# Optimization experiments

Measured on AMD Instinct MI355X. Metric: run time of the kernel, lower is better.

Reference implementation:

```python
import jax, jax.numpy as jnp
import numpy as np

EPS = 1e-5


def setup_inputs() -> dict:
    key = jax.random.key(0)
    ks = jax.random.split(key, 16)
    N, P, K, D = 16, 1024, 16, 3
    Cf = 64      # out_features (lifted feature dim)
    Fin = 64     # feature_dim
    Cout = 128   # out_channels
    DM = 4       # depth multiplier
    Ccat = Cf + Fin  # 128
    s = 0.1
    return {
        'rep_pt': jax.random.normal(ks[0], (N, P, D), jnp.float32),
        'pts':    jax.random.normal(ks[1], (N, P, K, D), jnp.float32),
        'fts':    jax.random.normal(ks[2], (N, P, K, Fin), jnp.float32),
        'W_fc1':  jax.random.normal(ks[3], (Cf, D), jnp.float32) * s,
        'b_fc1':  jnp.zeros((Cf,), jnp.float32),
        'W_fc2':  jax.random.normal(ks[4], (Cf, Cf), jnp.float32) * s,
        'b_fc2':  jnp.zeros((Cf,), jnp.float32),
        'W_xconv': jax.random.normal(ks[5], (K * K, D, K), jnp.float32) * s,
        'b_xconv': jnp.zeros((K * K,), jnp.float32),
        'W_xfc1': jax.random.normal(ks[6], (K * K, K * K), jnp.float32) * s,
        'b_xfc1': jnp.zeros((K * K,), jnp.float32),
        'W_xfc2': jax.random.normal(ks[7], (K * K, K * K), jnp.float32) * s,
        'b_xfc2': jnp.zeros((K * K,), jnp.float32),
        'W_dw':   jax.random.normal(ks[8], (Ccat, DM, K), jnp.float32) * s,
        'b_dw':   jnp.zeros((Ccat * DM,), jnp.float32),
        'W_pw':   jax.random.normal(ks[9], (Cout, Ccat * DM), jnp.float32) * s,
        'b_pw':   jnp.zeros((Cout,), jnp.float32),
        'gamma':  jnp.ones((Cout,), jnp.float32),
        'beta':   jnp.zeros((Cout,), jnp.float32),
    }


def reference(rep_pt, pts, fts, W_fc1, b_fc1, W_fc2, b_fc2,
              W_xconv, b_xconv, W_xfc1, b_xfc1, W_xfc2, b_xfc2,
              W_dw, b_dw, W_pw, b_pw, gamma, beta):
    relu = jax.nn.relu
    N, P, K, _ = pts.shape

    # local coords around each representative point
    pts_local = pts - rep_pt[:, :, None, :]                       # (N,P,K,3)

    # feature lift: two FCs with relu
    h = relu(jnp.einsum('npkd,fd->npkf', pts_local, W_fc1) + b_fc1)
    fts_lifted = relu(jnp.einsum('npkf,gf->npkg', h, W_fc2) + b_fc2)  # (N,P,K,Cf)
    fts_cat = jnp.concatenate([fts_lifted, fts], axis=-1)         # (N,P,K,Ccat)

    # X-transform: conv2d kernel (1,K) over (N,3,P,K) -> (N,K^2,P,1), then 2 FCs
    X = relu(jnp.einsum('npkd,odk->npo', pts_local, W_xconv) + b_xconv)  # (N,P,K^2)
    X = relu(X @ W_xfc1.T + b_xfc1)
    X = X @ W_xfc2.T + b_xfc2                                     # linear
    X = X.reshape(N, P, K, K)

    # X-transformed features
    fts_X = jnp.einsum('npij,npjc->npic', X, fts_cat)             # (N,P,K,Ccat)

    # depthwise-separable conv with kernel (1,K): reduces K entirely
    x = fts_X.transpose(0, 3, 1, 2)                               # (N,Ccat,P,K)
    dw = jnp.einsum('ncpk,cmk->ncmp', x, W_dw)                    # (N,Ccat,DM,P)
    dw = dw.reshape(N, -1, P) + b_dw[None, :, None]               # (N,Ccat*DM,P)
    y = jnp.einsum('ncp,oc->nop', dw, W_pw) + b_pw[None, :, None] # (N,Cout,P)

    # batchnorm (training stats over N,P per channel), then relu
    mean = y.mean(axis=(0, 2), keepdims=True)
    var = y.var(axis=(0, 2), keepdims=True)
    y = (y - mean) * jax.lax.rsqrt(var + EPS)
    y = relu(gamma[None, :, None] * y + beta[None, :, None])

    return y.transpose(0, 2, 1)                                   # (N,P,Cout)
```

## Files before the change

### kernel.cpp

```cpp
#include <hip/hip_runtime.h>


#define NPTS 16384

typedef short  s16x8 __attribute__((ext_vector_type(8)));
typedef float  f32x4 __attribute__((ext_vector_type(4)));

__device__ inline unsigned short f2b(float f) {
    unsigned u = __builtin_bit_cast(unsigned, f);
    unsigned r = u + 0x7FFF + ((u >> 16) & 1);
    return (unsigned short)(r >> 16);
}
__device__ inline float b2f(unsigned short b) {
    return __builtin_bit_cast(float, (unsigned)b << 16);
}
__device__ inline unsigned cvtpk(float lo, float hi) {
    unsigned r;
    asm("v_cvt_pk_bf16_f32 %0, %1, %2" : "=v"(r) : "v"(lo), "v"(hi));
    return r;
}

#define MFMA(a,b,c) __builtin_amdgcn_mfma_f32_16x16x32_bf16((a),(b),(c),0,0,0)

__global__ __launch_bounds__(256) void kW_cvt(
    const float* __restrict__ Wxc, const float* __restrict__ Wx1,
    const float* __restrict__ Wx2, const float* __restrict__ Wf2,
    const float* __restrict__ Wpw, const float* __restrict__ Wf1,
    const float* __restrict__ bf1, const float* __restrict__ Wdw,
    unsigned short* __restrict__ Wpk, float* __restrict__ W1p,
    unsigned short* __restrict__ Wtb, float* __restrict__ acc)
{
    unsigned short* Wxcpk = Wpk;
    unsigned short* Wx1pk = Wpk + 16384;
    unsigned short* Wx2pk = Wpk + 81920;
    unsigned short* Wf2pk = Wpk + 147456;
    unsigned short* Wpwpk = Wpk + 151552;
    int idx = blockIdx.x * 256 + threadIdx.x;
    if (idx < 16384) {
        int e = idx & 7, ln = (idx >> 3) & 63, ks = (idx >> 9) & 1, ot = idx >> 10;
        int row = ot*16 + (ln & 15), k = ks*32 + (ln >> 4)*8 + e;
        Wxcpk[idx] = (k < 48) ? f2b(Wxc[row*48 + k]) : 0; return; }
    idx -= 16384;
    if (idx < 65536) {
        int e = idx & 7, ln = (idx >> 3) & 63, ks = (idx >> 9) & 7, ot = idx >> 12;
        int row = ot*16 + (ln & 15), k = ks*32 + (ln >> 4)*8 + e;
        Wx1pk[idx] = f2b(Wx1[row*256 + k]); return; }
    idx -= 65536;
    if (idx < 65536) {
        int e = idx & 7, ln = (idx >> 3) & 63, ks = (idx >> 9) & 7, ot = idx >> 12;
        int row = ot*16 + (ln & 15), k = ks*32 + (ln >> 4)*8 + e;
        Wx2pk[idx] = f2b(Wx2[row*256 + k]); return; }
    idx -= 65536;
    if (idx < 4096) {
        int e = idx & 7, ln = (idx >> 3) & 63, ks = (idx >> 9) & 1, ot = idx >> 10;
        int row = ot*16 + (ln & 15), k = ks*32 + (ln >> 4)*8 + e;
        Wf2pk[idx] = f2b(Wf2[row*64 + k]); return; }
    idx -= 4096;
    if (idx < 65536) {
        int e = idx & 7, ln = (idx >> 3) & 63, ks = (idx >> 9) & 15, ot = idx >> 13;
        int row = ot*16 + (ln & 15), k = ks*32 + (ln >> 4)*8 + e;
        Wpwpk[idx] = f2b(Wpw[row*512 + k]); return; }
    idx -= 65536;
    if (idx < 256)   { int f = idx >> 2, j = idx & 3;
        W1p[idx] = (j < 3) ? Wf1[f*3 + j] : bf1[f]; return; }
    idx -= 256;
    if (idx < 8192)  { int m = idx >> 11, rem = idx & 2047;
        int c = rem >> 4, k = rem & 15;
        Wtb[idx] = f2b(Wdw[(size_t)(c*4 + m)*16 + k]); return; }
    idx -= 8192;
    if (idx < 256)   { acc[idx] = 0.f; return; }
}

#define SX 264
__global__ __launch_bounds__(512) void kA_mfma(
    const float* __restrict__ rep, const float* __restrict__ pts,
    const unsigned short* __restrict__ Wpk,
    const float* __restrict__ bxc, const float* __restrict__ bx1,
    const float* __restrict__ bx2, unsigned short* __restrict__ X3b)
{
    const unsigned short* Wxcpk = Wpk;
    const unsigned short* Wx1pk = Wpk + 16384;
    const unsigned short* Wx2pk = Wpk + 81920;
    __shared__ __align__(16) unsigned short X1s[32*SX];
    __shared__ __align__(16) unsigned short X2s[32*SX];
    const int tid = threadIdx.x;
    const int w = tid >> 6, lane = tid & 63, cl = lane & 15, lg = lane >> 4;
    const int mw = w & 1, nw = w >> 1;
    const int base = blockIdx.x * 32;
    const int q = base + mw*16 + cl;
    f32x4 z = {0.f,0.f,0.f,0.f};

    float r0 = rep[q*3+0], r1 = rep[q*3+1], r2 = rep[q*3+2];
    s16x8 aa[2];
    #pragma unroll
    for (int ks = 0; ks < 2; ++ks) {
        uint4 au;
        #pragma unroll
        for (int e2 = 0; e2 < 4; ++e2) {
            float v[2];
            #pragma unroll
            for (int h = 0; h < 2; ++h) {
                int j = ks*32 + lg*8 + e2*2 + h;
                float vv = 0.f;
                if (j < 48) {
                    int d = j >> 4, kk = j & 15;
                    float rv = (d == 0) ? r0 : ((d == 1) ? r1 : r2);
                    vv = pts[(size_t)(q*16 + kk)*3 + d] - rv;
                }
                v[h] = vv;
            }
            ((unsigned*)&au)[e2] = cvtpk(v[0], v[1]);
        }
        aa[ks] = __builtin_bit_cast(s16x8, au);
    }

    {
        f32x4 acc[4] = {z,z,z,z};
        #pragma unroll
        for (int ks = 0; ks < 2; ++ks) {
            #pragma unroll
            for (int ct = 0; ct < 4; ++ct) {
                int ot = nw*4 + ct;
                s16x8 b = *(const s16x8*)&Wxcpk[((ot*2 + ks)*64 + lane)*8];
                acc[ct] = MFMA(aa[ks], b, acc[ct]);
            }
        }
        #pragma unroll
        for (int ct = 0; ct < 4; ++ct) {
            int o = nw*64 + ct*16 + cl;
            float bias = bxc[o];
            int rb = (mw*16 + lg*4)*SX + o;
            unsigned u0 = cvtpk(fmaxf(acc[ct][0]+bias,0.f), fmaxf(acc[ct][1]+bias,0.f));
            unsigned u1 = cvtpk(fmaxf(acc[ct][2]+bias,0.f), fmaxf(acc[ct][3]+bias,0.f));
            X1s[rb       ] = (unsigned short)u0;
            X1s[rb +   SX] = (unsigned short)(u0 >> 16);
            X1s[rb + 2*SX] = (unsigned short)u1;
            X1s[rb + 3*SX] = (unsigned short)(u1 >> 16);
        }
    }
    __syncthreads();

    {
        f32x4 acc[4] = {z,z,z,z};
        #pragma unroll
        for (int ks = 0; ks < 8; ++ks) {
            s16x8 a = *(const s16x8*)&X1s[(mw*16 + cl)*SX + ks*32 + lg*8];
            #pragma unroll
            for (int ct = 0; ct < 4; ++ct) {
                int ot = nw*4 + ct;
                s16x8 b = *(const s16x8*)&Wx1pk[((ot*8 + ks)*64 + lane)*8];
                acc[ct] = MFMA(a, b, acc[ct]);
            }
        }
        #pragma unroll
        for (int ct = 0; ct < 4; ++ct) {
            int o = nw*64 + ct*16 + cl;
            float bias = bx1[o];
            int rb = (mw*16 + lg*4)*SX + o;
            unsigned u0 = cvtpk(fmaxf(acc[ct][0]+bias,0.f), fmaxf(acc[ct][1]+bias,0.f));
            unsigned u1 = cvtpk(fmaxf(acc[ct][2]+bias,0.f), fmaxf(acc[ct][3]+bias,0.f));
            X2s[rb       ] = (unsigned short)u0;
            X2s[rb +   SX] = (unsigned short)(u0 >> 16);
            X2s[rb + 2*SX] = (unsigned short)u1;
            X2s[rb + 3*SX] = (unsigned short)(u1 >> 16);
        }
    }
    __syncthreads();

    {
        f32x4 acc[4] = {z,z,z,z};
        #pragma unroll
        for (int ks = 0; ks < 8; ++ks) {
            s16x8 a = *(const s16x8*)&X2s[(mw*16 + cl)*SX + ks*32 + lg*8];
            #pragma unroll
            for (int ct = 0; ct < 4; ++ct) {
                int ot = nw*4 + ct;
                s16x8 b = *(const s16x8*)&Wx2pk[((ot*8 + ks)*64 + lane)*8];
                acc[ct] = MFMA(a, b, acc[ct]);
            }
        }
        #pragma unroll
        for (int ct = 0; ct < 4; ++ct) {
            int o = nw*64 + ct*16 + cl;
            float bias = bx2[o];
            size_t rb = (size_t)(base + mw*16 + lg*4)*256 + o;
            unsigned u0 = cvtpk(acc[ct][0]+bias, acc[ct][1]+bias);
            unsigned u1 = cvtpk(acc[ct][2]+bias, acc[ct][3]+bias);
            X3b[rb      ] = (unsigned short)u0;
            X3b[rb + 256] = (unsigned short)(u0 >> 16);
            X3b[rb + 512] = (unsigned short)u1;
            X3b[rb + 768] = (unsigned short)(u1 >> 16);
        }
    }
}

#define SF 72
__global__ __launch_bounds__(256) void kB_mfma(
    const float* __restrict__ rep, const float* __restrict__ pts,
    const float* __restrict__ fts, const float* __restrict__ W1p,
    const unsigned short* __restrict__ Wpk, const float* __restrict__ bf2,
    const unsigned short* __restrict__ Wtb, const float* __restrict__ bdw,
    const unsigned short* __restrict__ X3b, unsigned short* __restrict__ dwb)
{
    const unsigned short* Wf2pk = Wpk + 147456;
    __shared__ __align__(16) unsigned short fcT[128*SF];
    const int tid = threadIdx.x;
    const int w = tid >> 6, lane = tid & 63, cl = lane & 15, lg = lane >> 4;
    const int p = blockIdx.x*4 + w;
    const int rw = w*16;

    const int frow = lane >> 2, fch = lane & 3;
    float4 fv[4];
    #pragma unroll
    for (int it = 0; it < 4; ++it)
        fv[it] = *(const float4*)&fts[((size_t)p*16 + frow)*64 + fch*4 + it*16];

    s16x8 xa = {0,0,0,0,0,0,0,0};
    if (lg < 2) xa = *(const s16x8*)&X3b[(size_t)p*256 + cl*16 + lg*8];

    const int row = p*16 + cl;
    float x0 = pts[(size_t)row*3+0] - rep[p*3+0];
    float x1 = pts[(size_t)row*3+1] - rep[p*3+1];
    float x2 = pts[(size_t)row*3+2] - rep[p*3+2];

    s16x8 hb[2];
    #pragma unroll
    for (int ks = 0; ks < 2; ++ks) {
        uint4 hu;
        #pragma unroll
        for (int e2 = 0; e2 < 4; ++e2) {
            int f0 = ks*32 + lg*8 + e2*2;
            float4 wa = *(const float4*)&W1p[f0*4];
            float4 wb = *(const float4*)&W1p[(f0+1)*4];
            float h0 = fmaxf(wa.w + wa.x*x0 + wa.y*x1 + wa.z*x2, 0.f);
            float h1 = fmaxf(wb.w + wb.x*x0 + wb.y*x1 + wb.z*x2, 0.f);
            ((unsigned*)&hu)[e2] = cvtpk(h0, h1);
        }
        hb[ks] = __builtin_bit_cast(s16x8, hu);
    }

    #pragma unroll
    for (int it = 0; it < 4; ++it) {
        int c0 = fch*4 + it*16;
        unsigned u0 = cvtpk(fv[it].x, fv[it].y);
        unsigned u1 = cvtpk(fv[it].z, fv[it].w);
        int rb = (64 + c0)*SF + rw + frow;
        fcT[rb       ] = (unsigned short)u0;
        fcT[rb +   SF] = (unsigned short)(u0 >> 16);
        fcT[rb + 2*SF] = (unsigned short)u1;
        fcT[rb + 3*SF] = (unsigned short)(u1 >> 16);
    }

    f32x4 z = {0.f,0.f,0.f,0.f};
    {
        f32x4 acc2[4] = {z,z,z,z};
        #pragma unroll
        for (int ks = 0; ks < 2; ++ks) {
            #pragma unroll
            for (int gt = 0; gt < 4; ++gt) {
                s16x8 a = *(const s16x8*)&Wf2pk[((gt*2 + ks)*64 + lane)*8];
                acc2[gt] = MFMA(a, hb[ks], acc2[gt]);
            }
        }
        #pragma unroll
        for (int gt = 0; gt < 4; ++gt) {
            int g0 = gt*16 + lg*4;
            unsigned u0 = cvtpk(fmaxf(acc2[gt][0]+bf2[g0+0],0.f),
                                fmaxf(acc2[gt][1]+bf2[g0+1],0.f));
            unsigned u1 = cvtpk(fmaxf(acc2[gt][2]+bf2[g0+2],0.f),
                                fmaxf(acc2[gt][3]+bf2[g0+3],0.f));
            int rb = g0*SF + rw + cl;
            fcT[rb       ] = (unsigned short)u0;
            fcT[rb +   SF] = (unsigned short)(u0 >> 16);
            fcT[rb + 2*SF] = (unsigned short)u1;
            fcT[rb + 3*SF] = (unsigned short)(u1 >> 16);
        }
    }

    #pragma unroll
    for (int ct = 0; ct < 8; ++ct) {
        int c = ct*16 + cl;
        s16x8 b = *(const s16x8*)&fcT[c*SF + rw + (lg & 1)*8];
        f32x4 fx = MFMA(xa, b, z);

        float4 b4 = *(const float4*)&bdw[c*4];
        float om[4];
        #pragma unroll
        for (int m = 0; m < 4; ++m) {
            ushort4 wu = *(const ushort4*)&Wtb[m*2048 + c*16 + lg*4];
            float s = fx[0]*b2f(wu.x) + fx[1]*b2f(wu.y)
                    + fx[2]*b2f(wu.z) + fx[3]*b2f(wu.w);
            s += __shfl_xor(s, 16);
            s += __shfl_xor(s, 32);
            om[m] = s + ((const float*)&b4)[m];
        }
        if (lg == 0) {
            unsigned u0 = cvtpk(om[0], om[1]);
            unsigned u1 = cvtpk(om[2], om[3]);
            uint2 pk; pk.x = u0; pk.y = u1;
            *(uint2*)&dwb[(size_t)p*512 + c*4] = pk;
        }
    }
}

__global__ __launch_bounds__(256) void kC_mfma(
    const unsigned short* __restrict__ dwb, const unsigned short* __restrict__ Wpk,
    const float* __restrict__ bpw, float* __restrict__ y,
    float* __restrict__ accS, float* __restrict__ accS2)
{
    const unsigned short* Wpwpk = Wpk + 151552;
    const int tid = threadIdx.x;
    const int w = tid >> 6, lane = tid & 63, cl = lane & 15, lg = lane >> 4;
    const int m0 = blockIdx.x*32 + (w & 1)*16;
    const int nh = w >> 1;
    f32x4 z = {0.f,0.f,0.f,0.f};
    f32x4 acc[4] = {z,z,z,z};
    for (int ks = 0; ks < 16; ++ks) {
        s16x8 a = *(const s16x8*)&dwb[(size_t)(m0 + cl)*512 + ks*32 + lg*8];
        #pragma unroll
        for (int ct = 0; ct < 4; ++ct) {
            int ot = nh*4 + ct;
            s16x8 b = *(const s16x8*)&Wpwpk[((ot*16 + ks)*64 + lane)*8];
            acc[ct] = MFMA(a, b, acc[ct]);
        }
    }
    #pragma unroll
    for (int ct = 0; ct < 4; ++ct) {
        int o = nh*64 + ct*16 + cl;
        float bias = bpw[o];
        float s1 = 0.f, s2 = 0.f;
        #pragma unroll
        for (int r = 0; r < 4; ++r) {
            float v = acc[ct][r] + bias;
            y[(size_t)(m0 + lg*4 + r)*128 + o] = v;
            s1 += v; s2 += v*v;
        }
        s1 += __shfl_xor(s1, 16); s2 += __shfl_xor(s2, 16);
        s1 += __shfl_xor(s1, 32); s2 += __shfl_xor(s2, 32);
        if (lg == 0) {
            atomicAdd(accS + o, s1);
            atomicAdd(accS2 + o, s2);
        }
    }
}

__global__ __launch_bounds__(256) void kE_final(
    const float* __restrict__ y, const float* __restrict__ accS,
    const float* __restrict__ accS2, const float* __restrict__ gamma,
    const float* __restrict__ beta, float* __restrict__ out)
{
    __shared__ float stl[256];
    const int tid = threadIdx.x;
    if (tid < 128) {
        float mean = accS[tid] * (1.f/NPTS);
        float var  = accS2[tid] * (1.f/NPTS) - mean*mean;
        float rstd = rsqrtf(var + 1e-5f);
        float sc = gamma[tid] * rstd;
        stl[tid] = sc;
        stl[128 + tid] = beta[tid] - mean*sc;
    }
    __syncthreads();
    const int idx = blockIdx.x*256 + tid;
    float4 v = ((const float4*)y)[idx];
    int o0 = (idx & 31) << 2;
    float4 sc = *(const float4*)&stl[o0];
    float4 sh = *(const float4*)&stl[128 + o0];
    float4 r;
    r.x = fmaxf(v.x*sc.x + sh.x, 0.f);
    r.y = fmaxf(v.y*sc.y + sh.y, 0.f);
    r.z = fmaxf(v.z*sc.z + sh.z, 0.f);
    r.w = fmaxf(v.w*sc.w + sh.w, 0.f);
    ((float4*)out)[idx] = r;
}

extern "C" void kernel_launch(void* const* d_in, const int* in_sizes, int n_in,
                              void* d_out, int out_size, void* d_ws, size_t ws_size,
                              hipStream_t stream) {
    const float* rep  = (const float*)d_in[0];
    const float* pts  = (const float*)d_in[1];
    const float* fts  = (const float*)d_in[2];
    const float* Wf1  = (const float*)d_in[3];
    const float* bf1  = (const float*)d_in[4];
    const float* Wf2  = (const float*)d_in[5];
    const float* bf2  = (const float*)d_in[6];
    const float* Wxc  = (const float*)d_in[7];
    const float* bxc  = (const float*)d_in[8];
    const float* Wx1  = (const float*)d_in[9];
    const float* bx1  = (const float*)d_in[10];
    const float* Wx2  = (const float*)d_in[11];
    const float* bx2  = (const float*)d_in[12];
    const float* Wdw  = (const float*)d_in[13];
    const float* bdw  = (const float*)d_in[14];
    const float* Wpw  = (const float*)d_in[15];
    const float* bpw  = (const float*)d_in[16];
    const float* gam  = (const float*)d_in[17];
    const float* bet  = (const float*)d_in[18];

    unsigned short* X3b = (unsigned short*)d_ws;
    unsigned short* dwb = X3b + (size_t)NPTS*256;
    float* y   = (float*)(dwb + (size_t)NPTS*512);
    float* acc = y + (size_t)NPTS*128;
    unsigned short* Wpk = (unsigned short*)(acc + 256);
    float* W1p = (float*)(Wpk + 217088);
    unsigned short* Wtb = (unsigned short*)(W1p + 256);

    kW_cvt<<<882, 256, 0, stream>>>(Wxc, Wx1, Wx2, Wf2, Wpw, Wf1, bf1, Wdw,
                                    Wpk, W1p, Wtb, acc);
    kA_mfma<<<NPTS/32, 512, 0, stream>>>(rep, pts, Wpk, bxc, bx1, bx2, X3b);
    kB_mfma<<<NPTS/4, 256, 0, stream>>>(rep, pts, fts, W1p, Wpk, bf2, Wtb, bdw, X3b, dwb);
    kC_mfma<<<NPTS/32, 256, 0, stream>>>(dwb, Wpk, bpw, y, acc, acc + 128);
    kE_final<<<(NPTS*128/4)/256, 256, 0, stream>>>(y, acc, acc + 128, gam, bet, (float*)d_out);
}
```

Baseline: 116.8 us.

## Store depthwise output in MFMA-packed layout and pre-BN activations as bf16

kB now writes its depthwise result directly into the fragment-packed order kC consumes, so each lane of kC loads its A operand with one contiguous vector read. The intermediate y written by kC and read by kE is stored in bf16 instead of fp32, halving that round trip's memory traffic. Batch-norm statistics are still accumulated from fp32 values, but normalization is applied to bf16-rounded values, which adds rounding error.

```diff
diff --git a/kernel.cpp b/kernel.cpp
--- a/kernel.cpp
+++ b/kernel.cpp
@@ -200,7 +200,7 @@
     const float* __restrict__ fts, const float* __restrict__ W1p,
     const unsigned short* __restrict__ Wpk, const float* __restrict__ bf2,
     const unsigned short* __restrict__ Wtb, const float* __restrict__ bdw,
-    const unsigned short* __restrict__ X3b, unsigned short* __restrict__ dwb)
+    const unsigned short* __restrict__ X3b, unsigned short* __restrict__ dwPk)
 {
     const unsigned short* Wf2pk = Wpk + 147456;
     __shared__ __align__(16) unsigned short fcT[128*SF];
@@ -298,25 +298,28 @@
             unsigned u0 = cvtpk(om[0], om[1]);
             unsigned u1 = cvtpk(om[2], om[3]);
             uint2 pk; pk.x = u0; pk.y = u1;
-            *(uint2*)&dwb[(size_t)p*512 + c*4] = pk;
+            size_t a = ((((size_t)(p >> 4)*16 + ct*2 + (cl >> 3))*64
+                        + ((cl >> 1) & 3)*16 + (p & 15))*8 + (cl & 1)*4);
+            *(uint2*)&dwPk[a] = pk;
         }
     }
 }
 
 __global__ __launch_bounds__(256) void kC_mfma(
-    const unsigned short* __restrict__ dwb, const unsigned short* __restrict__ Wpk,
-    const float* __restrict__ bpw, float* __restrict__ y,
+    const unsigned short* __restrict__ dwPk, const unsigned short* __restrict__ Wpk,
+    const float* __restrict__ bpw, unsigned short* __restrict__ yb,
     float* __restrict__ accS, float* __restrict__ accS2)
 {
     const unsigned short* Wpwpk = Wpk + 151552;
     const int tid = threadIdx.x;
     const int w = tid >> 6, lane = tid & 63, cl = lane & 15, lg = lane >> 4;
-    const int m0 = blockIdx.x*32 + (w & 1)*16;
+    const int mt = blockIdx.x*2 + (w & 1);
+    const int m0 = mt*16;
     const int nh = w >> 1;
     f32x4 z = {0.f,0.f,0.f,0.f};
     f32x4 acc[4] = {z,z,z,z};
     for (int ks = 0; ks < 16; ++ks) {
-        s16x8 a = *(const s16x8*)&dwb[(size_t)(m0 + cl)*512 + ks*32 + lg*8];
+        s16x8 a = *(const s16x8*)&dwPk[(((size_t)mt*16 + ks)*64 + lane)*8];
         #pragma unroll
         for (int ct = 0; ct < 4; ++ct) {
             int ot = nh*4 + ct;
@@ -332,7 +335,7 @@
         #pragma unroll
         for (int r = 0; r < 4; ++r) {
             float v = acc[ct][r] + bias;
-            y[(size_t)(m0 + lg*4 + r)*128 + o] = v;
+            yb[(size_t)(m0 + lg*4 + r)*128 + o] = f2b(v);
             s1 += v; s2 += v*v;
         }
         s1 += __shfl_xor(s1, 16); s2 += __shfl_xor(s2, 16);
@@ -345,7 +348,7 @@
 }
 
 __global__ __launch_bounds__(256) void kE_final(
-    const float* __restrict__ y, const float* __restrict__ accS,
+    const unsigned short* __restrict__ yb, const float* __restrict__ accS,
     const float* __restrict__ accS2, const float* __restrict__ gamma,
     const float* __restrict__ beta, float* __restrict__ out)
 {
@@ -361,15 +364,15 @@
     }
     __syncthreads();
     const int idx = blockIdx.x*256 + tid;
-    float4 v = ((const float4*)y)[idx];
+    ushort4 u = *(const ushort4*)&yb[(size_t)idx*4];
     int o0 = (idx & 31) << 2;
     float4 sc = *(const float4*)&stl[o0];
     float4 sh = *(const float4*)&stl[128 + o0];
     float4 r;
-    r.x = fmaxf(v.x*sc.x + sh.x, 0.f);
-    r.y = fmaxf(v.y*sc.y + sh.y, 0.f);
-    r.z = fmaxf(v.z*sc.z + sh.z, 0.f);
-    r.w = fmaxf(v.w*sc.w + sh.w, 0.f);
+    r.x = fmaxf(b2f(u.x)*sc.x + sh.x, 0.f);
+    r.y = fmaxf(b2f(u.y)*sc.y + sh.y, 0.f);
+    r.z = fmaxf(b2f(u.z)*sc.z + sh.z, 0.f);
+    r.w = fmaxf(b2f(u.w)*sc.w + sh.w, 0.f);
     ((float4*)out)[idx] = r;
 }
 
@@ -396,10 +399,10 @@
     const float* gam  = (const float*)d_in[17];
     const float* bet  = (const float*)d_in[18];
 
-    unsigned short* X3b = (unsigned short*)d_ws;
-    unsigned short* dwb = X3b + (size_t)NPTS*256;
-    float* y   = (float*)(dwb + (size_t)NPTS*512);
-    float* acc = y + (size_t)NPTS*128;
+    unsigned short* X3b  = (unsigned short*)d_ws;
+    unsigned short* dwPk = X3b + (size_t)NPTS*256;
+    unsigned short* yb   = dwPk + (size_t)NPTS*512;
+    float* acc = (float*)(yb + (size_t)NPTS*128);
     unsigned short* Wpk = (unsigned short*)(acc + 256);
     float* W1p = (float*)(Wpk + 217088);
     unsigned short* Wtb = (unsigned short*)(W1p + 256);
@@ -407,7 +410,7 @@
     kW_cvt<<<882, 256, 0, stream>>>(Wxc, Wx1, Wx2, Wf2, Wpw, Wf1, bf1, Wdw,
                                     Wpk, W1p, Wtb, acc);
     kA_mfma<<<NPTS/32, 512, 0, stream>>>(rep, pts, Wpk, bxc, bx1, bx2, X3b);
-    kB_mfma<<<NPTS/4, 256, 0, stream>>>(rep, pts, fts, W1p, Wpk, bf2, Wtb, bdw, X3b, dwb);
-    kC_mfma<<<NPTS/32, 256, 0, stream>>>(dwb, Wpk, bpw, y, acc, acc + 128);
-    kE_final<<<(NPTS*128/4)/256, 256, 0, stream>>>(y, acc, acc + 128, gam, bet, (float*)d_out);
-}
+    kB_mfma<<<NPTS/4, 256, 0, stream>>>(rep, pts, fts, W1p, Wpk, bf2, Wtb, bdw, X3b, dwPk);
+    kC_mfma<<<NPTS/32, 256, 0, stream>>>(dwPk, Wpk, bpw, yb, acc, acc + 128);
+    kE_final<<<(NPTS*128/4)/256, 256, 0, stream>>>(yb, acc, acc + 128, gam, bet, (float*)d_out);
+}
```

After: 115.6 us. About the same (-1.0%).
